# Kernel optimization log

Hardware: AMD Instinct MI355X
Metric: run time of the kernel (lower is better)

## Reference

```python
import jax, jax.numpy as jnp
import numpy as np

B, T, E, H = 8, 2048, 1024, 64  # batch, seq_len(=block_size), embedding_size, head_size


def setup_inputs() -> dict:
    key = jax.random.key(0)
    k1, k2, k3, k4, k5 = jax.random.split(key, 5)
    x = jax.random.normal(k1, (B, T, E), dtype=jnp.float32)
    Wk = jax.random.normal(k2, (H, E), dtype=jnp.float32) * 0.02
    Wq = jax.random.normal(k3, (H, E), dtype=jnp.float32) * 0.02
    Wv = jax.random.normal(k4, (H, E), dtype=jnp.float32) * 0.02
    attention_mask = jax.random.randint(k5, (B, T), 0, 2).astype(jnp.int32)
    return {"x": x, "Wk": Wk, "Wq": Wq, "Wv": Wv, "attention_mask": attention_mask}


def reference(x, Wk, Wq, Wv, attention_mask):
    # Linear projections (nn.Linear with no bias: y = x @ W.T)
    k = jnp.einsum('bte,he->bth', x, Wk)
    q = jnp.einsum('bte,he->bth', x, Wq)
    v = jnp.einsum('bte,he->bth', x, Wv)
    scale = v.shape[2] ** -0.5  # head_size^-0.5, faithful to v.shape[2]**(-0.5)
    wei = jnp.einsum('bqh,bkh->bqk', q, k) * scale  # [B,T,T]
    # Causal mask (tril buffer) AND padding outer-product mask; the double-precision
    # outer product in the original just tests nonzero-ness, so a boolean AND is exact.
    causal = jnp.tril(jnp.ones((T, T), dtype=bool))  # [T,T]
    pad = (attention_mask[:, :, None] * attention_mask[:, None, :]) != 0  # [B,T,T]
    wei = jnp.where(causal[None, :, :] & pad, wei, -jnp.inf)
    wei = jax.nn.softmax(wei, axis=-1)
    wei = jnp.nan_to_num(wei)  # fully-masked rows -> 0 (matches torch.nan_to_num)
    # dropout in eval mode -> identity
    out = jnp.einsum('bqk,bkh->bqh', wei, v)
    return out
```

## Files before the change

kernel.cpp:

```cpp
#include <hip/hip_runtime.h>
#include <hip/hip_bf16.h>

typedef __bf16 bf16x8 __attribute__((ext_vector_type(8)));
typedef __bf16 bf16x4 __attribute__((ext_vector_type(4)));
typedef float  f32x4  __attribute__((ext_vector_type(4)));

#define LDP 72

#define BAR() { asm volatile("s_waitcnt lgkmcnt(0)" ::: "memory"); __builtin_amdgcn_s_barrier(); }

__global__ __launch_bounds__(256) void wconv_kernel(
    const float* __restrict__ Wk, const float* __restrict__ Wq,
    const float* __restrict__ Wv, __bf16* __restrict__ wbf)
{
    int idx = blockIdx.x * 256 + threadIdx.x;
    int row = idx >> 8;
    int c4  = idx & 255;
    const float* wp = (row < 64) ? Wk + (size_t)row * 1024
                    : (row < 128) ? Wq + (size_t)(row - 64) * 1024
                                  : Wv + (size_t)(row - 128) * 1024;
    float4 f = *reinterpret_cast<const float4*>(wp + c4 * 4);
    bf16x4 v; v[0] = (__bf16)f.x; v[1] = (__bf16)f.y; v[2] = (__bf16)f.z; v[3] = (__bf16)f.w;
    *reinterpret_cast<bf16x4*>(&wbf[(size_t)row * 1024 + c4 * 4]) = v;
}

__global__ __launch_bounds__(512) void maskpack_kernel(
    const int* __restrict__ mask, unsigned* __restrict__ maskw)
{
    int wdx = threadIdx.x;
    unsigned wv = 0;
    #pragma unroll
    for (int bit = 0; bit < 32; bit++)
        wv |= (mask[wdx * 32 + bit] != 0 ? 1u : 0u) << bit;
    maskw[wdx] = wv;
}

__global__ __launch_bounds__(1024) void proj_kernel(
    const float* __restrict__ x, const __bf16* __restrict__ wbf,
    __bf16* __restrict__ kbuf, __bf16* __restrict__ qbuf, __bf16* __restrict__ vtbuf)
{
    __shared__ __align__(16) __bf16 Slds[2][256 * LDP];
    __shared__ __align__(16) __bf16 Vtl[64 * LDP];

    const int tid  = threadIdx.x;
    const int lane = tid & 63;
    const int wid  = tid >> 6;
    const int wm   = wid >> 2;
    const int wn   = wid & 3;
    const int mbase = blockIdx.x * 64;

    const int cl = lane & 15;
    const int e0 = (lane >> 4) * 8;
    const int r0 = (lane >> 4) * 4;

    const int arow = tid >> 4, acg = tid & 15;
    const float* aptr = x + (size_t)(mbase + arow) * 1024 + acg * 4;

    float4 a0, a1;
    bf16x4 w0[3], w1[3];

#define ISSUE(aset, wset, kb) { \
    aset = *reinterpret_cast<const float4*>(aptr + (kb)); \
    _Pragma("unroll") \
    for (int i_ = 0; i_ < 3; i_++) { \
        int c_ = i_ * 1024 + tid; \
        wset[i_] = *reinterpret_cast<const bf16x4*>(&wbf[(size_t)(c_ >> 4) * 1024 + (kb) + (c_ & 15) * 4]); \
    } }

#define COMMIT(aset, wset, bufi) { \
    bf16x4 av_; \
    av_[0] = (__bf16)aset.x; av_[1] = (__bf16)aset.y; av_[2] = (__bf16)aset.z; av_[3] = (__bf16)aset.w; \
    *reinterpret_cast<bf16x4*>(&Slds[bufi][arow * LDP + acg * 4]) = av_; \
    _Pragma("unroll") \
    for (int i_ = 0; i_ < 3; i_++) { \
        int c_ = i_ * 1024 + tid; \
        *reinterpret_cast<bf16x4*>(&Slds[bufi][(64 + (c_ >> 4)) * LDP + (c_ & 15) * 4]) = wset[i_]; \
    } }

    f32x4 acc[3];
    #pragma unroll
    for (int n = 0; n < 3; n++) acc[n] = (f32x4){0.f, 0.f, 0.f, 0.f};

    ISSUE(a0, w0, 0);
    COMMIT(a0, w0, 0);
    ISSUE(a1, w1, 64);
    BAR();

    #pragma unroll 2
    for (int j = 0; j < 16; j++) {
        if (j < 14) {
            if (j & 1) { ISSUE(a1, w1, (j + 2) * 64); }
            else       { ISSUE(a0, w0, (j + 2) * 64); }
        }
        const __bf16* buf = Slds[j & 1];
        #pragma unroll
        for (int kk = 0; kk < 2; kk++) {
            bf16x8 a = *reinterpret_cast<const bf16x8*>(&buf[(wm * 16 + cl) * LDP + kk * 32 + e0]);
            #pragma unroll
            for (int nf = 0; nf < 3; nf++) {
                bf16x8 b = *reinterpret_cast<const bf16x8*>(&buf[(64 + wn * 48 + nf * 16 + cl) * LDP + kk * 32 + e0]);
                acc[nf] = __builtin_amdgcn_mfma_f32_16x16x32_bf16(a, b, acc[nf], 0, 0, 0);
            }
        }
        if (j < 15) {
            if (j & 1) { COMMIT(a0, w0, 0); }
            else       { COMMIT(a1, w1, 1); }
            BAR();
        }
    }
#undef ISSUE
#undef COMMIT

    #pragma unroll
    for (int nf = 0; nf < 3; nf++) {
        int c = wn * 48 + nf * 16 + cl;
        #pragma unroll
        for (int r = 0; r < 4; r++) {
            int mrel = wm * 16 + r0 + r;
            float v = acc[nf][r];
            if (c < 64)        kbuf[(size_t)(mbase + mrel) * 64 + c]         = (__bf16)v;
            else if (c < 128)  qbuf[(size_t)(mbase + mrel) * 64 + (c - 64)]  = (__bf16)v;
            else               Vtl[(c - 128) * LDP + mrel]                   = (__bf16)v;
        }
    }
    __syncthreads();
    {
        int b   = mbase >> 11;
        int tof = mbase & 2047;
        int h   = tid >> 4;
        int seg = tid & 15;
        bf16x4 v4 = *reinterpret_cast<const bf16x4*>(&Vtl[h * LDP + seg * 4]);
        *reinterpret_cast<bf16x4*>(&vtbuf[(size_t)b * 64 * 2048 + (size_t)h * 2048 + tof + seg * 4]) = v4;
    }
}

__global__ __launch_bounds__(256) void attn_kernel(
    const __bf16* __restrict__ qbuf, const __bf16* __restrict__ kbuf,
    const __bf16* __restrict__ vtbuf, const unsigned* __restrict__ maskw,
    const int* __restrict__ mask,
    float* __restrict__ out, float* __restrict__ accpart, float* __restrict__ mlpart,
    int nsplit, int tps)
{
    __shared__ __align__(16) __bf16 Klds[64 * LDP];
    __shared__ __align__(16) __bf16 Vlds[64 * LDP];
    __shared__ __align__(16) __bf16 Plds[4][16 * LDP];

    const int tid  = threadIdx.x;
    const int lane = tid & 63;
    const int w    = tid >> 6;
    const int qt   = blockIdx.x;
    const int sp   = blockIdx.y;
    const int b    = blockIdx.z;
    const int qbase = qt * 64 + w * 16;

    const int jbeg = sp * tps;
    const int jend = min((sp + 1) * tps, qt + 1);

    if (nsplit > 1 && jbeg >= jend) {
        float* ap = accpart + ((size_t)(b * nsplit + sp) * 2048 + qt * 64) * 64;
        for (int i = tid; i < 64 * 64; i += 256) ap[i] = 0.f;
        float* mp = mlpart + ((size_t)(b * nsplit + sp) * 2048 + qt * 64) * 2;
        for (int i = tid; i < 64; i += 256) { mp[2 * i] = -INFINITY; mp[2 * i + 1] = 0.f; }
        return;
    }

    const int cl = lane & 15;
    const int e0 = (lane >> 4) * 8;
    const int r0 = (lane >> 4) * 4;
    const int qs = qbase + cl;

    bf16x8 aq[2];
    #pragma unroll
    for (int kk = 0; kk < 2; kk++)
        aq[kk] = *reinterpret_cast<const bf16x8*>(&qbuf[((size_t)b * 2048 + qs) * 64 + kk * 32 + e0]);

    float m = -INFINITY, l = 0.f;
    f32x4 acc[4];
    #pragma unroll
    for (int hf = 0; hf < 4; hf++) acc[hf] = (f32x4){0.f, 0.f, 0.f, 0.f};

    const int srow = tid >> 3;
    const int scg  = tid & 7;

    bf16x8 k0, k1, v0, v1;

#define KV_ISSUE(jj) { \
    size_t kb_ = ((size_t)b * 2048 + (jj) * 64 + srow) * 64 + scg * 8; \
    k0 = *reinterpret_cast<const bf16x8*>(&kbuf[kb_]); \
    k1 = *reinterpret_cast<const bf16x8*>(&kbuf[kb_ + (size_t)32 * 64]); \
    size_t vb_ = (size_t)b * 64 * 2048 + (size_t)srow * 2048 + (jj) * 64 + scg * 8; \
    v0 = *reinterpret_cast<const bf16x8*>(&vtbuf[vb_]); \
    v1 = *reinterpret_cast<const bf16x8*>(&vtbuf[vb_ + (size_t)32 * 2048]); }

#define KV_COMMIT() { \
    *reinterpret_cast<bf16x8*>(&Klds[srow * LDP + scg * 8]) = k0; \
    *reinterpret_cast<bf16x8*>(&Klds[(32 + srow) * LDP + scg * 8]) = k1; \
    *reinterpret_cast<bf16x8*>(&Vlds[srow * LDP + scg * 8]) = v0; \
    *reinterpret_cast<bf16x8*>(&Vlds[(32 + srow) * LDP + scg * 8]) = v1; }

    const int nt = jend - jbeg;
    KV_ISSUE(jbeg);
    KV_COMMIT();
    BAR();

    for (int t = 0; t < nt; t++) {
        const int j = jbeg + t;
        if (t + 1 < nt) KV_ISSUE(j + 1);

        f32x4 s[4];
        #pragma unroll
        for (int jf = 0; jf < 4; jf++) {
            f32x4 tacc = (f32x4){0.f, 0.f, 0.f, 0.f};
            #pragma unroll
            for (int kk = 0; kk < 2; kk++) {
                bf16x8 bk = *reinterpret_cast<const bf16x8*>(&Klds[(jf * 16 + cl) * LDP + kk * 32 + e0]);
                tacc = __builtin_amdgcn_mfma_f32_16x16x32_bf16(bk, aq[kk], tacc, 0, 0, 0);
            }
            s[jf] = tacc;
        }

        const unsigned mw0 = maskw[b * 64 + j * 2];
        const unsigned mw1 = maskw[b * 64 + j * 2 + 1];
        float tmax = -INFINITY;
        #pragma unroll
        for (int jf = 0; jf < 4; jf++) {
            unsigned mw = (jf < 2) ? mw0 : mw1;
            #pragma unroll
            for (int r = 0; r < 4; r++) {
                int kvl = jf * 16 + r0 + r;
                bool ok = ((mw >> (kvl & 31)) & 1u) && (j * 64 + kvl <= qs);
                float sv = s[jf][r] * 0.125f;
                sv = ok ? sv : -INFINITY;
                s[jf][r] = sv;
                tmax = fmaxf(tmax, sv);
            }
        }
        tmax = fmaxf(tmax, __shfl_xor(tmax, 16));
        tmax = fmaxf(tmax, __shfl_xor(tmax, 32));

        float mn = fmaxf(m, tmax);
        float alpha = (mn == -INFINITY) ? 1.0f : __expf(m - mn);
        float rs = 0.f;
        #pragma unroll
        for (int jf = 0; jf < 4; jf++)
            #pragma unroll
            for (int r = 0; r < 4; r++) {
                float p = (mn == -INFINITY) ? 0.f : __expf(s[jf][r] - mn);
                s[jf][r] = p;
                rs += p;
            }
        rs += __shfl_xor(rs, 16);
        rs += __shfl_xor(rs, 32);
        l = l * alpha + rs;
        m = mn;

        #pragma unroll
        for (int r = 0; r < 4; r++) {
            float ar = __shfl(alpha, r0 + r);
            #pragma unroll
            for (int hf = 0; hf < 4; hf++) acc[hf][r] *= ar;
        }

        #pragma unroll
        for (int jf = 0; jf < 4; jf++) {
            bf16x4 p4;
            #pragma unroll
            for (int r = 0; r < 4; r++) p4[r] = (__bf16)s[jf][r];
            *reinterpret_cast<bf16x4*>(&Plds[w][cl * LDP + jf * 16 + r0]) = p4;
        }
        #pragma unroll
        for (int kk = 0; kk < 2; kk++) {
            bf16x8 ap = *reinterpret_cast<const bf16x8*>(&Plds[w][cl * LDP + kk * 32 + e0]);
            #pragma unroll
            for (int hf = 0; hf < 4; hf++) {
                bf16x8 bv = *reinterpret_cast<const bf16x8*>(&Vlds[(hf * 16 + cl) * LDP + kk * 32 + e0]);
                acc[hf] = __builtin_amdgcn_mfma_f32_16x16x32_bf16(ap, bv, acc[hf], 0, 0, 0);
            }
        }

        BAR();
        if (t + 1 < nt) {
            KV_COMMIT();
            BAR();
        }
    }
#undef KV_ISSUE
#undef KV_COMMIT

    if (nsplit == 1) {
        #pragma unroll
        for (int r = 0; r < 4; r++) {
            int qrow = qbase + r0 + r;
            float lq = __shfl(l, r0 + r);
            int mq = mask[b * 2048 + qrow];
            #pragma unroll
            for (int hf = 0; hf < 4; hf++) {
                float v = (lq > 0.f && mq != 0) ? acc[hf][r] / lq : 0.f;
                out[((size_t)b * 2048 + qrow) * 64 + hf * 16 + cl] = v;
            }
        }
    } else {
        #pragma unroll
        for (int hf = 0; hf < 4; hf++)
            #pragma unroll
            for (int r = 0; r < 4; r++) {
                int qrow = qbase + r0 + r;
                accpart[((size_t)(b * nsplit + sp) * 2048 + qrow) * 64 + hf * 16 + cl] = acc[hf][r];
            }
        if (lane < 16) {
            int qrow = qbase + lane;
            mlpart[((size_t)(b * nsplit + sp) * 2048 + qrow) * 2 + 0] = m;
            mlpart[((size_t)(b * nsplit + sp) * 2048 + qrow) * 2 + 1] = l;
        }
    }
}

template<int NS>
__global__ __launch_bounds__(256) void combine_kernel(
    const float* __restrict__ accpart, const float* __restrict__ mlpart,
    const int* __restrict__ mask, float* __restrict__ out)
{
    int idx = blockIdx.x * 256 + threadIdx.x;
    int qglob = idx >> 6;
    int h = idx & 63;
    int b = qglob >> 11;
    int qrow = qglob & 2047;

    if (mask[qglob] == 0) { out[idx] = 0.f; return; }

    float m_s[NS], l_s[NS];
    float M = -INFINITY;
    #pragma unroll
    for (int s = 0; s < NS; s++) {
        size_t mo = ((size_t)(b * NS + s) * 2048 + qrow) * 2;
        m_s[s] = mlpart[mo];
        l_s[s] = mlpart[mo + 1];
        M = fmaxf(M, m_s[s]);
    }
    if (M == -INFINITY) { out[idx] = 0.f; return; }

    float L = 0.f, O = 0.f;
    #pragma unroll
    for (int s = 0; s < NS; s++) {
        float wgt = (m_s[s] == -INFINITY) ? 0.f : __expf(m_s[s] - M);
        L += l_s[s] * wgt;
        O += wgt * accpart[((size_t)(b * NS + s) * 2048 + qrow) * 64 + h];
    }
    out[idx] = (L > 0.f) ? O / L : 0.f;
}

extern "C" void kernel_launch(void* const* d_in, const int* in_sizes, int n_in,
                              void* d_out, int out_size, void* d_ws, size_t ws_size,
                              hipStream_t stream) {
    const float* x  = (const float*)d_in[0];
    const float* Wk = (const float*)d_in[1];
    const float* Wq = (const float*)d_in[2];
    const float* Wv = (const float*)d_in[3];
    const int* mask = (const int*)d_in[4];
    float* out = (float*)d_out;

    const size_t NTOK = 8 * 2048;
    __bf16* kbuf  = (__bf16*)d_ws;
    __bf16* qbuf  = kbuf + NTOK * 64;
    __bf16* vtbuf = qbuf + NTOK * 64;
    __bf16* wbf   = vtbuf + (size_t)8 * 64 * 2048;
    unsigned* maskw = (unsigned*)(wbf + (size_t)192 * 1024);
    const size_t base_bytes = NTOK * 64 * 2 * 2 + (size_t)8 * 64 * 2048 * 2
                            + (size_t)192 * 1024 * 2 + 512 * 4;

    const size_t acc_per_split = NTOK * 64 * 4;
    const size_t ml_per_split  = NTOK * 2 * 4;
    int nsplit = 1;
    if (ws_size >= base_bytes + 4 * (acc_per_split + ml_per_split))      nsplit = 4;
    else if (ws_size >= base_bytes + 2 * (acc_per_split + ml_per_split)) nsplit = 2;

    float* accpart = (float*)((char*)d_ws + base_bytes);
    float* mlpart  = accpart + NTOK * 64 * nsplit;

    wconv_kernel<<<192, 256, 0, stream>>>(Wk, Wq, Wv, wbf);
    maskpack_kernel<<<1, 512, 0, stream>>>(mask, maskw);
    proj_kernel<<<256, 1024, 0, stream>>>(x, wbf, kbuf, qbuf, vtbuf);
    attn_kernel<<<dim3(32, nsplit, 8), 256, 0, stream>>>(
        qbuf, kbuf, vtbuf, maskw, mask, out, accpart, mlpart, nsplit, 32 / nsplit);
    if (nsplit == 4)
        combine_kernel<4><<<(16384 * 64) / 256, 256, 0, stream>>>(accpart, mlpart, mask, out);
    else if (nsplit == 2)
        combine_kernel<2><<<(16384 * 64) / 256, 256, 0, stream>>>(accpart, mlpart, mask, out);
}
```

Before: 60.87 us.

## Load K/V fragments directly from global into registers, drop LDS staging and barriers

Measured after the change: 87.66 us. +44.0%, slower.

```diff
diff --git a/kernel.cpp b/kernel.cpp
--- a/kernel.cpp
+++ b/kernel.cpp
@@ -141,16 +141,16 @@
     float* __restrict__ out, float* __restrict__ accpart, float* __restrict__ mlpart,
     int nsplit, int tps)
 {
-    __shared__ __align__(16) __bf16 Klds[64 * LDP];
-    __shared__ __align__(16) __bf16 Vlds[64 * LDP];
     __shared__ __align__(16) __bf16 Plds[4][16 * LDP];
 
     const int tid  = threadIdx.x;
     const int lane = tid & 63;
     const int w    = tid >> 6;
-    const int qt   = blockIdx.x;
-    const int sp   = blockIdx.y;
-    const int b    = blockIdx.z;
+    const int wg   = blockIdx.x;
+    const int b    = wg & 7;
+    const int rr_  = wg >> 3;
+    const int qt   = rr_ & 31;
+    const int sp   = rr_ >> 5;
     const int qbase = qt * 64 + w * 16;
 
     const int jbeg = sp * tps;
@@ -179,113 +179,102 @@
     #pragma unroll
     for (int hf = 0; hf < 4; hf++) acc[hf] = (f32x4){0.f, 0.f, 0.f, 0.f};
 
-    const int srow = tid >> 3;
-    const int scg  = tid & 7;
-
-    bf16x8 k0, k1, v0, v1;
-
-#define KV_ISSUE(jj) { \
-    size_t kb_ = ((size_t)b * 2048 + (jj) * 64 + srow) * 64 + scg * 8; \
-    k0 = *reinterpret_cast<const bf16x8*>(&kbuf[kb_]); \
-    k1 = *reinterpret_cast<const bf16x8*>(&kbuf[kb_ + (size_t)32 * 64]); \
-    size_t vb_ = (size_t)b * 64 * 2048 + (size_t)srow * 2048 + (jj) * 64 + scg * 8; \
-    v0 = *reinterpret_cast<const bf16x8*>(&vtbuf[vb_]); \
-    v1 = *reinterpret_cast<const bf16x8*>(&vtbuf[vb_ + (size_t)32 * 2048]); }
-
-#define KV_COMMIT() { \
-    *reinterpret_cast<bf16x8*>(&Klds[srow * LDP + scg * 8]) = k0; \
-    *reinterpret_cast<bf16x8*>(&Klds[(32 + srow) * LDP + scg * 8]) = k1; \
-    *reinterpret_cast<bf16x8*>(&Vlds[srow * LDP + scg * 8]) = v0; \
-    *reinterpret_cast<bf16x8*>(&Vlds[(32 + srow) * LDP + scg * 8]) = v1; }
+    const __bf16* kb = kbuf + (size_t)b * 2048 * 64;
+    const __bf16* vtb = vtbuf + (size_t)b * 64 * 2048;
+
+    bf16x8 kfA[8], kfB[8], vf[8];
+
+#define KLOAD(dst, jj) { \
+    _Pragma("unroll") \
+    for (int f_ = 0; f_ < 8; f_++) { \
+        int jf_ = f_ >> 1, kk_ = f_ & 1; \
+        dst[f_] = *reinterpret_cast<const bf16x8*>(&kb[(size_t)((jj) * 64 + jf_ * 16 + cl) * 64 + kk_ * 32 + e0]); \
+    } }
+
+#define VLOAD(dst, jj) { \
+    _Pragma("unroll") \
+    for (int f_ = 0; f_ < 8; f_++) { \
+        int hf_ = f_ >> 1, kk_ = f_ & 1; \
+        dst[f_] = *reinterpret_cast<const bf16x8*>(&vtb[(size_t)(hf_ * 16 + cl) * 2048 + (jj) * 64 + kk_ * 32 + e0]); \
+    } }
+
+#define TILE_BODY(KFC, KFN) { \
+     \
+    f32x4 s[4]; \
+    _Pragma("unroll") \
+    for (int jf = 0; jf < 4; jf++) { \
+        f32x4 tacc = (f32x4){0.f, 0.f, 0.f, 0.f}; \
+        _Pragma("unroll") \
+        for (int kk = 0; kk < 2; kk++) \
+            tacc = __builtin_amdgcn_mfma_f32_16x16x32_bf16(KFC[jf * 2 + kk], aq[kk], tacc, 0, 0, 0); \
+        s[jf] = tacc; \
+    } \
+    VLOAD(vf, j);                      \
+    const unsigned mw0 = maskw[b * 64 + j * 2]; \
+    const unsigned mw1 = maskw[b * 64 + j * 2 + 1]; \
+    float tmax = -INFINITY; \
+    _Pragma("unroll") \
+    for (int jf = 0; jf < 4; jf++) { \
+        unsigned mw = (jf < 2) ? mw0 : mw1; \
+        _Pragma("unroll") \
+        for (int r = 0; r < 4; r++) { \
+            int kvl = jf * 16 + r0 + r; \
+            bool ok = ((mw >> (kvl & 31)) & 1u) && (j * 64 + kvl <= qs); \
+            float sv = s[jf][r] * 0.125f; \
+            sv = ok ? sv : -INFINITY; \
+            s[jf][r] = sv; \
+            tmax = fmaxf(tmax, sv); \
+        } \
+    } \
+    tmax = fmaxf(tmax, __shfl_xor(tmax, 16)); \
+    tmax = fmaxf(tmax, __shfl_xor(tmax, 32)); \
+    float mn = fmaxf(m, tmax); \
+    float alpha = (mn == -INFINITY) ? 1.0f : __expf(m - mn); \
+    float rs = 0.f; \
+    _Pragma("unroll") \
+    for (int jf = 0; jf < 4; jf++) \
+        _Pragma("unroll") \
+        for (int r = 0; r < 4; r++) { \
+            float p = (mn == -INFINITY) ? 0.f : __expf(s[jf][r] - mn); \
+            s[jf][r] = p; \
+            rs += p; \
+        } \
+    rs += __shfl_xor(rs, 16); \
+    rs += __shfl_xor(rs, 32); \
+    l = l * alpha + rs; \
+    m = mn; \
+    if (t + 1 < nt) KLOAD(KFN, j + 1);    \
+    _Pragma("unroll") \
+    for (int r = 0; r < 4; r++) { \
+        float ar = __shfl(alpha, r0 + r); \
+        _Pragma("unroll") \
+        for (int hf = 0; hf < 4; hf++) acc[hf][r] *= ar; \
+    } \
+    _Pragma("unroll") \
+    for (int jf = 0; jf < 4; jf++) { \
+        bf16x4 p4; \
+        _Pragma("unroll") \
+        for (int r = 0; r < 4; r++) p4[r] = (__bf16)s[jf][r]; \
+        *reinterpret_cast<bf16x4*>(&Plds[w][cl * LDP + jf * 16 + r0]) = p4; \
+    } \
+    _Pragma("unroll") \
+    for (int kk = 0; kk < 2; kk++) { \
+        bf16x8 ap = *reinterpret_cast<const bf16x8*>(&Plds[w][cl * LDP + kk * 32 + e0]); \
+        _Pragma("unroll") \
+        for (int hf = 0; hf < 4; hf++) \
+            acc[hf] = __builtin_amdgcn_mfma_f32_16x16x32_bf16(ap, vf[hf * 2 + kk], acc[hf], 0, 0, 0); \
+    } }
 
     const int nt = jend - jbeg;
-    KV_ISSUE(jbeg);
-    KV_COMMIT();
-    BAR();
-
+    KLOAD(kfA, jbeg);
     for (int t = 0; t < nt; t++) {
         const int j = jbeg + t;
-        if (t + 1 < nt) KV_ISSUE(j + 1);
-
-        f32x4 s[4];
-        #pragma unroll
-        for (int jf = 0; jf < 4; jf++) {
-            f32x4 tacc = (f32x4){0.f, 0.f, 0.f, 0.f};
-            #pragma unroll
-            for (int kk = 0; kk < 2; kk++) {
-                bf16x8 bk = *reinterpret_cast<const bf16x8*>(&Klds[(jf * 16 + cl) * LDP + kk * 32 + e0]);
-                tacc = __builtin_amdgcn_mfma_f32_16x16x32_bf16(bk, aq[kk], tacc, 0, 0, 0);
-            }
-            s[jf] = tacc;
-        }
-
-        const unsigned mw0 = maskw[b * 64 + j * 2];
-        const unsigned mw1 = maskw[b * 64 + j * 2 + 1];
-        float tmax = -INFINITY;
-        #pragma unroll
-        for (int jf = 0; jf < 4; jf++) {
-            unsigned mw = (jf < 2) ? mw0 : mw1;
-            #pragma unroll
-            for (int r = 0; r < 4; r++) {
-                int kvl = jf * 16 + r0 + r;
-                bool ok = ((mw >> (kvl & 31)) & 1u) && (j * 64 + kvl <= qs);
-                float sv = s[jf][r] * 0.125f;
-                sv = ok ? sv : -INFINITY;
-                s[jf][r] = sv;
-                tmax = fmaxf(tmax, sv);
-            }
-        }
-        tmax = fmaxf(tmax, __shfl_xor(tmax, 16));
-        tmax = fmaxf(tmax, __shfl_xor(tmax, 32));
-
-        float mn = fmaxf(m, tmax);
-        float alpha = (mn == -INFINITY) ? 1.0f : __expf(m - mn);
-        float rs = 0.f;
-        #pragma unroll
-        for (int jf = 0; jf < 4; jf++)
-            #pragma unroll
-            for (int r = 0; r < 4; r++) {
-                float p = (mn == -INFINITY) ? 0.f : __expf(s[jf][r] - mn);
-                s[jf][r] = p;
-                rs += p;
-            }
-        rs += __shfl_xor(rs, 16);
-        rs += __shfl_xor(rs, 32);
-        l = l * alpha + rs;
-        m = mn;
-
-        #pragma unroll
-        for (int r = 0; r < 4; r++) {
-            float ar = __shfl(alpha, r0 + r);
-            #pragma unroll
-            for (int hf = 0; hf < 4; hf++) acc[hf][r] *= ar;
-        }
-
-        #pragma unroll
-        for (int jf = 0; jf < 4; jf++) {
-            bf16x4 p4;
-            #pragma unroll
-            for (int r = 0; r < 4; r++) p4[r] = (__bf16)s[jf][r];
-            *reinterpret_cast<bf16x4*>(&Plds[w][cl * LDP + jf * 16 + r0]) = p4;
-        }
-        #pragma unroll
-        for (int kk = 0; kk < 2; kk++) {
-            bf16x8 ap = *reinterpret_cast<const bf16x8*>(&Plds[w][cl * LDP + kk * 32 + e0]);
-            #pragma unroll
-            for (int hf = 0; hf < 4; hf++) {
-                bf16x8 bv = *reinterpret_cast<const bf16x8*>(&Vlds[(hf * 16 + cl) * LDP + kk * 32 + e0]);
-                acc[hf] = __builtin_amdgcn_mfma_f32_16x16x32_bf16(ap, bv, acc[hf], 0, 0, 0);
-            }
-        }
-
-        BAR();
-        if (t + 1 < nt) {
-            KV_COMMIT();
-            BAR();
-        }
-    }
-#undef KV_ISSUE
-#undef KV_COMMIT
+        if (t & 1) { TILE_BODY(kfB, kfA); }
+        else       { TILE_BODY(kfA, kfB); }
+    }
+#undef KLOAD
+#undef VLOAD
+#undef TILE_BODY
 
     if (nsplit == 1) {
         #pragma unroll
@@ -380,7 +369,7 @@
     wconv_kernel<<<192, 256, 0, stream>>>(Wk, Wq, Wv, wbf);
     maskpack_kernel<<<1, 512, 0, stream>>>(mask, maskw);
     proj_kernel<<<256, 1024, 0, stream>>>(x, wbf, kbuf, qbuf, vtbuf);
-    attn_kernel<<<dim3(32, nsplit, 8), 256, 0, stream>>>(
+    attn_kernel<<<8 * 32 * nsplit, 256, 0, stream>>>(
         qbuf, kbuf, vtbuf, maskw, mask, out, accpart, mlpart, nsplit, 32 / nsplit);
     if (nsplit == 4)
         combine_kernel<4><<<(16384 * 64) / 256, 256, 0, stream>>>(accpart, mlpart, mask, out);
```

## Double-buffer K/V tiles with 32-key blocks and a flattened batch-major grid

Applied to the files above, without the earlier changes.

Result: slower. 64.43 us (+5.8%).

```diff
diff --git a/kernel.cpp b/kernel.cpp
--- a/kernel.cpp
+++ b/kernel.cpp
@@ -6,6 +6,8 @@
 typedef float  f32x4  __attribute__((ext_vector_type(4)));
 
 #define LDP 72
+#define KLDP 72
+#define VLDP 40
 
 #define BAR() { asm volatile("s_waitcnt lgkmcnt(0)" ::: "memory"); __builtin_amdgcn_s_barrier(); }
 
@@ -141,20 +143,22 @@
     float* __restrict__ out, float* __restrict__ accpart, float* __restrict__ mlpart,
     int nsplit, int tps)
 {
-    __shared__ __align__(16) __bf16 Klds[64 * LDP];
-    __shared__ __align__(16) __bf16 Vlds[64 * LDP];
-    __shared__ __align__(16) __bf16 Plds[4][16 * LDP];
+    __shared__ __align__(16) __bf16 Klds[2][32 * KLDP];
+    __shared__ __align__(16) __bf16 Vlds[2][64 * VLDP];
+    __shared__ __align__(16) __bf16 Plds[4][16 * VLDP];
 
     const int tid  = threadIdx.x;
     const int lane = tid & 63;
     const int w    = tid >> 6;
-    const int qt   = blockIdx.x;
-    const int sp   = blockIdx.y;
-    const int b    = blockIdx.z;
+    const int wg   = blockIdx.x;
+    const int b    = wg & 7;
+    const int rr_  = wg >> 3;
+    const int qt   = rr_ & 31;
+    const int sp   = rr_ >> 5;
     const int qbase = qt * 64 + w * 16;
 
     const int jbeg = sp * tps;
-    const int jend = min((sp + 1) * tps, qt + 1);
+    const int jend = min((sp + 1) * tps, 2 * qt + 2);
 
     if (nsplit > 1 && jbeg >= jend) {
         float* ap = accpart + ((size_t)(b * nsplit + sp) * 2048 + qt * 64) * 64;
@@ -179,62 +183,59 @@
     #pragma unroll
     for (int hf = 0; hf < 4; hf++) acc[hf] = (f32x4){0.f, 0.f, 0.f, 0.f};
 
-    const int srow = tid >> 3;
-    const int scg  = tid & 7;
-
-    bf16x8 k0, k1, v0, v1;
+    const __bf16* kb  = kbuf  + (size_t)b * 2048 * 64;
+    const __bf16* vtb = vtbuf + (size_t)b * 64 * 2048;
+
+    const int krow = tid >> 3, kcg = tid & 7;
+    const int vrow = tid >> 2, vcg = tid & 3;
+    bf16x8 st_k, st_v;
 
 #define KV_ISSUE(jj) { \
-    size_t kb_ = ((size_t)b * 2048 + (jj) * 64 + srow) * 64 + scg * 8; \
-    k0 = *reinterpret_cast<const bf16x8*>(&kbuf[kb_]); \
-    k1 = *reinterpret_cast<const bf16x8*>(&kbuf[kb_ + (size_t)32 * 64]); \
-    size_t vb_ = (size_t)b * 64 * 2048 + (size_t)srow * 2048 + (jj) * 64 + scg * 8; \
-    v0 = *reinterpret_cast<const bf16x8*>(&vtbuf[vb_]); \
-    v1 = *reinterpret_cast<const bf16x8*>(&vtbuf[vb_ + (size_t)32 * 2048]); }
-
-#define KV_COMMIT() { \
-    *reinterpret_cast<bf16x8*>(&Klds[srow * LDP + scg * 8]) = k0; \
-    *reinterpret_cast<bf16x8*>(&Klds[(32 + srow) * LDP + scg * 8]) = k1; \
-    *reinterpret_cast<bf16x8*>(&Vlds[srow * LDP + scg * 8]) = v0; \
-    *reinterpret_cast<bf16x8*>(&Vlds[(32 + srow) * LDP + scg * 8]) = v1; }
+    st_k = *reinterpret_cast<const bf16x8*>(&kb[(size_t)((jj) * 32 + krow) * 64 + kcg * 8]); \
+    st_v = *reinterpret_cast<const bf16x8*>(&vtb[(size_t)vrow * 2048 + (jj) * 32 + vcg * 8]); }
+
+#define KV_COMMIT(bi) { \
+    *reinterpret_cast<bf16x8*>(&Klds[bi][krow * KLDP + kcg * 8]) = st_k; \
+    *reinterpret_cast<bf16x8*>(&Vlds[bi][vrow * VLDP + vcg * 8]) = st_v; }
 
     const int nt = jend - jbeg;
     KV_ISSUE(jbeg);
-    KV_COMMIT();
+    KV_COMMIT(0);
+    if (nt > 1) KV_ISSUE(jbeg + 1);
     BAR();
 
     for (int t = 0; t < nt; t++) {
         const int j = jbeg + t;
-        if (t + 1 < nt) KV_ISSUE(j + 1);
-
-        f32x4 s[4];
-        #pragma unroll
-        for (int jf = 0; jf < 4; jf++) {
+        const int cur = t & 1;
+
+        if (t + 1 < nt) KV_COMMIT(cur ^ 1);
+        if (t + 2 < nt) KV_ISSUE(j + 2);
+
+        f32x4 s[2];
+        #pragma unroll
+        for (int jf = 0; jf < 2; jf++) {
             f32x4 tacc = (f32x4){0.f, 0.f, 0.f, 0.f};
             #pragma unroll
             for (int kk = 0; kk < 2; kk++) {
-                bf16x8 bk = *reinterpret_cast<const bf16x8*>(&Klds[(jf * 16 + cl) * LDP + kk * 32 + e0]);
+                bf16x8 bk = *reinterpret_cast<const bf16x8*>(&Klds[cur][(jf * 16 + cl) * KLDP + kk * 32 + e0]);
                 tacc = __builtin_amdgcn_mfma_f32_16x16x32_bf16(bk, aq[kk], tacc, 0, 0, 0);
             }
             s[jf] = tacc;
         }
 
-        const unsigned mw0 = maskw[b * 64 + j * 2];
-        const unsigned mw1 = maskw[b * 64 + j * 2 + 1];
+        const unsigned mw = maskw[b * 64 + j];
         float tmax = -INFINITY;
         #pragma unroll
-        for (int jf = 0; jf < 4; jf++) {
-            unsigned mw = (jf < 2) ? mw0 : mw1;
+        for (int jf = 0; jf < 2; jf++)
             #pragma unroll
             for (int r = 0; r < 4; r++) {
                 int kvl = jf * 16 + r0 + r;
-                bool ok = ((mw >> (kvl & 31)) & 1u) && (j * 64 + kvl <= qs);
+                bool ok = ((mw >> kvl) & 1u) && (j * 32 + kvl <= qs);
                 float sv = s[jf][r] * 0.125f;
                 sv = ok ? sv : -INFINITY;
                 s[jf][r] = sv;
                 tmax = fmaxf(tmax, sv);
             }
-        }
         tmax = fmaxf(tmax, __shfl_xor(tmax, 16));
         tmax = fmaxf(tmax, __shfl_xor(tmax, 32));
 
@@ -242,7 +243,7 @@
         float alpha = (mn == -INFINITY) ? 1.0f : __expf(m - mn);
         float rs = 0.f;
         #pragma unroll
-        for (int jf = 0; jf < 4; jf++)
+        for (int jf = 0; jf < 2; jf++)
             #pragma unroll
             for (int r = 0; r < 4; r++) {
                 float p = (mn == -INFINITY) ? 0.f : __expf(s[jf][r] - mn);
@@ -255,58 +256,46 @@
         m = mn;
 
         #pragma unroll
-        for (int r = 0; r < 4; r++) {
-            float ar = __shfl(alpha, r0 + r);
-            #pragma unroll
-            for (int hf = 0; hf < 4; hf++) acc[hf][r] *= ar;
-        }
-
-        #pragma unroll
-        for (int jf = 0; jf < 4; jf++) {
+        for (int hf = 0; hf < 4; hf++)
+            #pragma unroll
+            for (int r = 0; r < 4; r++) acc[hf][r] *= alpha;
+
+        #pragma unroll
+        for (int jf = 0; jf < 2; jf++) {
             bf16x4 p4;
             #pragma unroll
             for (int r = 0; r < 4; r++) p4[r] = (__bf16)s[jf][r];
-            *reinterpret_cast<bf16x4*>(&Plds[w][cl * LDP + jf * 16 + r0]) = p4;
-        }
-        #pragma unroll
-        for (int kk = 0; kk < 2; kk++) {
-            bf16x8 ap = *reinterpret_cast<const bf16x8*>(&Plds[w][cl * LDP + kk * 32 + e0]);
+            *reinterpret_cast<bf16x4*>(&Plds[w][cl * VLDP + jf * 16 + r0]) = p4;
+        }
+        {
+            bf16x8 pb = *reinterpret_cast<const bf16x8*>(&Plds[w][cl * VLDP + e0]);
             #pragma unroll
             for (int hf = 0; hf < 4; hf++) {
-                bf16x8 bv = *reinterpret_cast<const bf16x8*>(&Vlds[(hf * 16 + cl) * LDP + kk * 32 + e0]);
-                acc[hf] = __builtin_amdgcn_mfma_f32_16x16x32_bf16(ap, bv, acc[hf], 0, 0, 0);
-            }
-        }
-
-        BAR();
-        if (t + 1 < nt) {
-            KV_COMMIT();
-            BAR();
-        }
+                bf16x8 av = *reinterpret_cast<const bf16x8*>(&Vlds[cur][(hf * 16 + cl) * VLDP + e0]);
+                acc[hf] = __builtin_amdgcn_mfma_f32_16x16x32_bf16(av, pb, acc[hf], 0, 0, 0);
+            }
+        }
+
+        if (t + 1 < nt) BAR();
     }
 #undef KV_ISSUE
 #undef KV_COMMIT
 
     if (nsplit == 1) {
-        #pragma unroll
-        for (int r = 0; r < 4; r++) {
-            int qrow = qbase + r0 + r;
-            float lq = __shfl(l, r0 + r);
-            int mq = mask[b * 2048 + qrow];
-            #pragma unroll
-            for (int hf = 0; hf < 4; hf++) {
-                float v = (lq > 0.f && mq != 0) ? acc[hf][r] / lq : 0.f;
-                out[((size_t)b * 2048 + qrow) * 64 + hf * 16 + cl] = v;
-            }
-        }
+        int mq = mask[b * 2048 + qs];
+        #pragma unroll
+        for (int hf = 0; hf < 4; hf++)
+            #pragma unroll
+            for (int r = 0; r < 4; r++) {
+                float v = (l > 0.f && mq != 0) ? acc[hf][r] / l : 0.f;
+                out[((size_t)b * 2048 + qs) * 64 + hf * 16 + r0 + r] = v;
+            }
     } else {
         #pragma unroll
         for (int hf = 0; hf < 4; hf++)
             #pragma unroll
-            for (int r = 0; r < 4; r++) {
-                int qrow = qbase + r0 + r;
-                accpart[((size_t)(b * nsplit + sp) * 2048 + qrow) * 64 + hf * 16 + cl] = acc[hf][r];
-            }
+            for (int r = 0; r < 4; r++)
+                accpart[((size_t)(b * nsplit + sp) * 2048 + qs) * 64 + hf * 16 + r0 + r] = acc[hf][r];
         if (lane < 16) {
             int qrow = qbase + lane;
             mlpart[((size_t)(b * nsplit + sp) * 2048 + qrow) * 2 + 0] = m;
@@ -380,8 +369,8 @@
     wconv_kernel<<<192, 256, 0, stream>>>(Wk, Wq, Wv, wbf);
     maskpack_kernel<<<1, 512, 0, stream>>>(mask, maskw);
     proj_kernel<<<256, 1024, 0, stream>>>(x, wbf, kbuf, qbuf, vtbuf);
-    attn_kernel<<<dim3(32, nsplit, 8), 256, 0, stream>>>(
-        qbuf, kbuf, vtbuf, maskw, mask, out, accpart, mlpart, nsplit, 32 / nsplit);
+    attn_kernel<<<8 * 32 * nsplit, 256, 0, stream>>>(
+        qbuf, kbuf, vtbuf, maskw, mask, out, accpart, mlpart, nsplit, 64 / nsplit);
     if (nsplit == 4)
         combine_kernel<4><<<(16384 * 64) / 256, 256, 0, stream>>>(accpart, mlpart, mask, out);
     else if (nsplit == 2)
```
